# Kernel tuning notes

Measured on AMD Instinct MI355X. Metric: run time of the kernel, lower is better.

## Reference

```python
import jax, jax.numpy as jnp
import numpy as np

B, V, D = 4096, 10000, 512
ANNEAL = 1.0
EPSILON = 1.0  # regularization_type = 'OT'


def setup_inputs() -> dict:
    key = jax.random.key(0)
    ks = jax.random.split(key, 8)
    return {
        "recon_x": jax.random.normal(ks[0], (B, V), dtype=jnp.float32),
        "logits_rec": jax.random.normal(ks[1], (B, V), dtype=jnp.float32),
        "logits_text": jax.random.normal(ks[2], (B, V), dtype=jnp.float32),
        "x": jax.random.uniform(ks[3], (B, V), dtype=jnp.float32),
        "mu": jax.random.normal(ks[4], (B, D), dtype=jnp.float32),
        "logvar": jax.random.normal(ks[5], (B, D), dtype=jnp.float32),
        "prior_mu": jax.random.normal(ks[6], (B, D), dtype=jnp.float32),
        "prior_logvar": jax.random.normal(ks[7], (B, D), dtype=jnp.float32),
    }


def _bce(logits, x):
    # -mean_b(mean_v(log_softmax(logits,1) * x)) == global mean since both
    # reductions are plain means over the full [B, V] tensor.
    return -jnp.mean(jax.nn.log_softmax(logits, axis=1) * x)


def _kld(m, lv):
    return -0.5 * jnp.mean(1.0 + lv - m * m - jnp.exp(lv))


def reference(recon_x, logits_rec, logits_text, x, mu, logvar, prior_mu, prior_logvar):
    BCE_merged = _bce(recon_x, x)
    BCE_text = _bce(logits_text, x)
    BCE_rec = _bce(logits_rec, x)
    BCE = (BCE_merged + BCE_text + BCE_rec) / 3.0

    KLD1 = _kld(mu, logvar)
    KLD2 = _kld(prior_mu, prior_logvar)

    # Bures-Wasserstein^2 between diagonal Gaussians. The torch code builds
    # dense diag matrices and runs batched Cholesky/bmm; for diagonal covs
    # L1 = diag(sqrt(s1)), L1 @ C2 @ L1^T = diag(s1*s2), chol -> diag(sqrt(s1*s2)),
    # so the math reduces exactly to the O(d) closed form below.
    s1 = jnp.exp(logvar)          # [B, D]
    s2 = jnp.exp(prior_logvar)    # [B, D]
    mean_dist_sq = jnp.sum((mu - prior_mu) ** 2, axis=1)            # [B]
    trace_term = jnp.sum(s1 + s2 - 2.0 * jnp.sqrt(s1 * s2), axis=1)  # [B]
    wasserstein_loss = jnp.mean(mean_dist_sq + trace_term)

    l = BCE + ANNEAL / 2.0 * (KLD1 + KLD2) + EPSILON * wasserstein_loss
    return (l, BCE, wasserstein_loss, BCE_rec, BCE_text, BCE_merged)
```

## Files before the change

kernel.cpp:

```cpp
#include <hip/hip_runtime.h>

#define NROWS 4096
#define NCOLS 10000
#define DDIM  512

__device__ __forceinline__ float wave_reduce_sum(float v) {
    #pragma unroll
    for (int o = 32; o > 0; o >>= 1) v += __shfl_down(v, o, 64);
    return v;
}

__global__ __launch_bounds__(256) void bce_rows_kernel(
    const float4* __restrict__ merged,
    const float4* __restrict__ rec,
    const float4* __restrict__ text,
    const float4* __restrict__ xr,
    float* __restrict__ cm, float* __restrict__ ct, float* __restrict__ cr)
{
    const int row = blockIdx.x;
    const int nvec = NCOLS / 4;
    const size_t base = (size_t)row * nvec;

    float se_m = 0.f, se_t = 0.f, se_r = 0.f;
    float d_m = 0.f, d_t = 0.f, d_r = 0.f;
    float sx = 0.f;

    for (int i = threadIdx.x; i < nvec; i += 256) {
        const float4 xv = xr[base + i];
        const float4 mv = merged[base + i];
        const float4 tv = text[base + i];
        const float4 rv = rec[base + i];

        se_m += __expf(mv.x) + __expf(mv.y) + __expf(mv.z) + __expf(mv.w);
        se_t += __expf(tv.x) + __expf(tv.y) + __expf(tv.z) + __expf(tv.w);
        se_r += __expf(rv.x) + __expf(rv.y) + __expf(rv.z) + __expf(rv.w);

        d_m += mv.x * xv.x + mv.y * xv.y + mv.z * xv.z + mv.w * xv.w;
        d_t += tv.x * xv.x + tv.y * xv.y + tv.z * xv.z + tv.w * xv.w;
        d_r += rv.x * xv.x + rv.y * xv.y + rv.z * xv.z + rv.w * xv.w;

        sx += xv.x + xv.y + xv.z + xv.w;
    }

    __shared__ float sm[4][7];
    float vals[7] = {se_m, se_t, se_r, d_m, d_t, d_r, sx};
    #pragma unroll
    for (int k = 0; k < 7; ++k) vals[k] = wave_reduce_sum(vals[k]);

    const int wave = threadIdx.x >> 6;
    const int lane = threadIdx.x & 63;
    if (lane == 0) {
        #pragma unroll
        for (int k = 0; k < 7; ++k) sm[wave][k] = vals[k];
    }
    __syncthreads();

    if (threadIdx.x == 0) {
        float t[7];
        #pragma unroll
        for (int k = 0; k < 7; ++k)
            t[k] = sm[0][k] + sm[1][k] + sm[2][k] + sm[3][k];
        const float sumx = t[6];
        cm[row] = t[3] - __logf(t[0]) * sumx;
        ct[row] = t[4] - __logf(t[1]) * sumx;
        cr[row] = t[5] - __logf(t[2]) * sumx;
    }
}

__global__ __launch_bounds__(256) void kld_wass_kernel(
    const float4* __restrict__ mu, const float4* __restrict__ lv,
    const float4* __restrict__ pmu, const float4* __restrict__ plv,
    float* __restrict__ k1o, float* __restrict__ k2o, float* __restrict__ wo)
{
    const int nvec = NROWS * DDIM / 4;
    float k1 = 0.f, k2 = 0.f, wacc = 0.f;

    for (int i = blockIdx.x * 256 + threadIdx.x; i < nvec; i += gridDim.x * 256) {
        const float4 m  = mu[i];
        const float4 l  = lv[i];
        const float4 pm = pmu[i];
        const float4 pl = plv[i];

        #define KW_COMP(c)                                              \
        {                                                               \
            const float e1 = __expf(l.c);                               \
            const float e2 = __expf(pl.c);                              \
            k1 += 1.f + l.c - m.c * m.c - e1;                           \
            k2 += 1.f + pl.c - pm.c * pm.c - e2;                        \
            const float dm = m.c - pm.c;                                \
            wacc += dm * dm + e1 + e2 - 2.f * __expf(0.5f * (l.c + pl.c)); \
        }
        KW_COMP(x) KW_COMP(y) KW_COMP(z) KW_COMP(w)
        #undef KW_COMP
    }

    __shared__ float sm[4][3];
    k1 = wave_reduce_sum(k1);
    k2 = wave_reduce_sum(k2);
    wacc = wave_reduce_sum(wacc);
    const int wave = threadIdx.x >> 6;
    const int lane = threadIdx.x & 63;
    if (lane == 0) { sm[wave][0] = k1; sm[wave][1] = k2; sm[wave][2] = wacc; }
    __syncthreads();
    if (threadIdx.x == 0) {
        k1o[blockIdx.x] = sm[0][0] + sm[1][0] + sm[2][0] + sm[3][0];
        k2o[blockIdx.x] = sm[0][1] + sm[1][1] + sm[2][1] + sm[3][1];
        wo[blockIdx.x]  = sm[0][2] + sm[1][2] + sm[2][2] + sm[3][2];
    }
}

__global__ __launch_bounds__(256) void finalize_kernel(
    const float* __restrict__ cm, const float* __restrict__ ct,
    const float* __restrict__ cr, const float* __restrict__ k1p,
    const float* __restrict__ k2p, const float* __restrict__ wp,
    int nk, float* __restrict__ out)
{
    float sm_ = 0.f, st_ = 0.f, sr_ = 0.f;
    for (int i = threadIdx.x; i < NROWS; i += 256) {
        sm_ += cm[i]; st_ += ct[i]; sr_ += cr[i];
    }
    float s1 = 0.f, s2 = 0.f, sw = 0.f;
    for (int i = threadIdx.x; i < nk; i += 256) {
        s1 += k1p[i]; s2 += k2p[i]; sw += wp[i];
    }

    __shared__ float sh[4][6];
    float vals[6] = {sm_, st_, sr_, s1, s2, sw};
    #pragma unroll
    for (int k = 0; k < 6; ++k) vals[k] = wave_reduce_sum(vals[k]);
    const int wave = threadIdx.x >> 6;
    const int lane = threadIdx.x & 63;
    if (lane == 0) {
        #pragma unroll
        for (int k = 0; k < 6; ++k) sh[wave][k] = vals[k];
    }
    __syncthreads();

    if (threadIdx.x == 0) {
        float t[6];
        #pragma unroll
        for (int k = 0; k < 6; ++k)
            t[k] = sh[0][k] + sh[1][k] + sh[2][k] + sh[3][k];

        const float invBV = 1.f / ((float)NROWS * (float)NCOLS);
        const float BCE_merged = -t[0] * invBV;
        const float BCE_text   = -t[1] * invBV;
        const float BCE_rec    = -t[2] * invBV;
        const float BCE = (BCE_merged + BCE_text + BCE_rec) * (1.f / 3.f);

        const float invBD = 1.f / ((float)NROWS * (float)DDIM);
        const float KLD1 = -0.5f * t[3] * invBD;
        const float KLD2 = -0.5f * t[4] * invBD;
        const float wass = t[5] / (float)NROWS;

        const float l = BCE + 0.5f * (KLD1 + KLD2) + wass;

        out[0] = l;
        out[1] = BCE;
        out[2] = wass;
        out[3] = BCE_rec;
        out[4] = BCE_text;
        out[5] = BCE_merged;
    }
}

extern "C" void kernel_launch(void* const* d_in, const int* in_sizes, int n_in,
                              void* d_out, int out_size, void* d_ws, size_t ws_size,
                              hipStream_t stream) {
    const float4* recon_x      = (const float4*)d_in[0];
    const float4* logits_rec   = (const float4*)d_in[1];
    const float4* logits_text  = (const float4*)d_in[2];
    const float4* x            = (const float4*)d_in[3];
    const float4* mu           = (const float4*)d_in[4];
    const float4* logvar       = (const float4*)d_in[5];
    const float4* prior_mu     = (const float4*)d_in[6];
    const float4* prior_logvar = (const float4*)d_in[7];

    float* ws = (float*)d_ws;
    float* cm = ws;
    float* ct = ws + NROWS;
    float* cr = ws + 2 * NROWS;
    const int NK = 512;
    float* k1p = ws + 3 * NROWS;
    float* k2p = ws + 3 * NROWS + NK;
    float* wp  = ws + 3 * NROWS + 2 * NK;

    hipLaunchKernelGGL(kld_wass_kernel, dim3(NK), dim3(256), 0, stream,
                       mu, logvar, prior_mu, prior_logvar, k1p, k2p, wp);
    hipLaunchKernelGGL(bce_rows_kernel, dim3(NROWS), dim3(256), 0, stream,
                       recon_x, logits_rec, logits_text, x, cm, ct, cr);
    hipLaunchKernelGGL(finalize_kernel, dim3(1), dim3(256), 0, stream,
                       cm, ct, cr, k1p, k2p, wp, NK, (float*)d_out);
}
```

Baseline: 133.5 us.

## Fuse KLD/Wasserstein and BCE kernels into one launch with unrolled row loop

The separate KLD/Wasserstein reduction kernel is merged into the BCE row kernel: the first 256 blocks do the KLD/Wasserstein partials and the remaining blocks do one row each. This removes one kernel launch and lets the small reduction overlap with the large streaming work. The BCE loop is unrolled by two so each thread has eight float4 loads in flight. The KLD block count also drops from 512 to 256, giving each of those blocks more work.

```diff
diff --git a/kernel.cpp b/kernel.cpp
--- a/kernel.cpp
+++ b/kernel.cpp
@@ -3,6 +3,7 @@
 #define NROWS 4096
 #define NCOLS 10000
 #define DDIM  512
+#define NKLD  256
 
 __device__ __forceinline__ float wave_reduce_sum(float v) {
     #pragma unroll
@@ -10,14 +11,57 @@
     return v;
 }
 
-__global__ __launch_bounds__(256) void bce_rows_kernel(
+__global__ __launch_bounds__(256) void fused_main_kernel(
     const float4* __restrict__ merged,
     const float4* __restrict__ rec,
     const float4* __restrict__ text,
     const float4* __restrict__ xr,
-    float* __restrict__ cm, float* __restrict__ ct, float* __restrict__ cr)
+    const float4* __restrict__ mu, const float4* __restrict__ lv,
+    const float4* __restrict__ pmu, const float4* __restrict__ plv,
+    float* __restrict__ cm, float* __restrict__ ct, float* __restrict__ cr,
+    float* __restrict__ k1o, float* __restrict__ k2o, float* __restrict__ wo)
 {
-    const int row = blockIdx.x;
+    const int wave = threadIdx.x >> 6;
+    const int lane = threadIdx.x & 63;
+
+    if (blockIdx.x < NKLD) {
+        const int nvec = NROWS * DDIM / 4;
+        float k1 = 0.f, k2 = 0.f, wacc = 0.f;
+
+        for (int i = blockIdx.x * 256 + threadIdx.x; i < nvec; i += NKLD * 256) {
+            const float4 m  = mu[i];
+            const float4 l  = lv[i];
+            const float4 pm = pmu[i];
+            const float4 pl = plv[i];
+
+            #define KW_COMP(c)                                              \
+            {                                                               \
+                const float e1 = __expf(l.c);                               \
+                const float e2 = __expf(pl.c);                              \
+                k1 += 1.f + l.c - m.c * m.c - e1;                           \
+                k2 += 1.f + pl.c - pm.c * pm.c - e2;                        \
+                const float dm = m.c - pm.c;                                \
+                wacc += dm * dm + e1 + e2 - 2.f * __expf(0.5f * (l.c + pl.c)); \
+            }
+            KW_COMP(x) KW_COMP(y) KW_COMP(z) KW_COMP(w)
+            #undef KW_COMP
+        }
+
+        __shared__ float sm[4][3];
+        k1 = wave_reduce_sum(k1);
+        k2 = wave_reduce_sum(k2);
+        wacc = wave_reduce_sum(wacc);
+        if (lane == 0) { sm[wave][0] = k1; sm[wave][1] = k2; sm[wave][2] = wacc; }
+        __syncthreads();
+        if (threadIdx.x == 0) {
+            k1o[blockIdx.x] = sm[0][0] + sm[1][0] + sm[2][0] + sm[3][0];
+            k2o[blockIdx.x] = sm[0][1] + sm[1][1] + sm[2][1] + sm[3][1];
+            wo[blockIdx.x]  = sm[0][2] + sm[1][2] + sm[2][2] + sm[3][2];
+        }
+        return;
+    }
+
+    const int row = blockIdx.x - NKLD;
     const int nvec = NCOLS / 4;
     const size_t base = (size_t)row * nvec;
 
@@ -25,33 +69,46 @@
     float d_m = 0.f, d_t = 0.f, d_r = 0.f;
     float sx = 0.f;
 
-    for (int i = threadIdx.x; i < nvec; i += 256) {
+    #define BCE_BODY(xv, mv, tv, rv)                                          \
+    {                                                                         \
+        se_m += __expf(mv.x) + __expf(mv.y) + __expf(mv.z) + __expf(mv.w);    \
+        se_t += __expf(tv.x) + __expf(tv.y) + __expf(tv.z) + __expf(tv.w);    \
+        se_r += __expf(rv.x) + __expf(rv.y) + __expf(rv.z) + __expf(rv.w);    \
+        d_m += mv.x * xv.x + mv.y * xv.y + mv.z * xv.z + mv.w * xv.w;         \
+        d_t += tv.x * xv.x + tv.y * xv.y + tv.z * xv.z + tv.w * xv.w;         \
+        d_r += rv.x * xv.x + rv.y * xv.y + rv.z * xv.z + rv.w * xv.w;         \
+        sx  += xv.x + xv.y + xv.z + xv.w;                                     \
+    }
+
+    int i = threadIdx.x;
+    for (; i + 256 < nvec; i += 512) {
+        const float4 xv0 = xr[base + i];
+        const float4 mv0 = merged[base + i];
+        const float4 tv0 = text[base + i];
+        const float4 rv0 = rec[base + i];
+        const float4 xv1 = xr[base + i + 256];
+        const float4 mv1 = merged[base + i + 256];
+        const float4 tv1 = text[base + i + 256];
+        const float4 rv1 = rec[base + i + 256];
+        BCE_BODY(xv0, mv0, tv0, rv0)
+        BCE_BODY(xv1, mv1, tv1, rv1)
+    }
+    for (; i < nvec; i += 256) {
         const float4 xv = xr[base + i];
         const float4 mv = merged[base + i];
         const float4 tv = text[base + i];
         const float4 rv = rec[base + i];
-
-        se_m += __expf(mv.x) + __expf(mv.y) + __expf(mv.z) + __expf(mv.w);
-        se_t += __expf(tv.x) + __expf(tv.y) + __expf(tv.z) + __expf(tv.w);
-        se_r += __expf(rv.x) + __expf(rv.y) + __expf(rv.z) + __expf(rv.w);
-
-        d_m += mv.x * xv.x + mv.y * xv.y + mv.z * xv.z + mv.w * xv.w;
-        d_t += tv.x * xv.x + tv.y * xv.y + tv.z * xv.z + tv.w * xv.w;
-        d_r += rv.x * xv.x + rv.y * xv.y + rv.z * xv.z + rv.w * xv.w;
-
-        sx += xv.x + xv.y + xv.z + xv.w;
-    }
-
-    __shared__ float sm[4][7];
+        BCE_BODY(xv, mv, tv, rv)
+    }
+    #undef BCE_BODY
+
+    __shared__ float sm2[4][7];
     float vals[7] = {se_m, se_t, se_r, d_m, d_t, d_r, sx};
     #pragma unroll
     for (int k = 0; k < 7; ++k) vals[k] = wave_reduce_sum(vals[k]);
-
-    const int wave = threadIdx.x >> 6;
-    const int lane = threadIdx.x & 63;
     if (lane == 0) {
         #pragma unroll
-        for (int k = 0; k < 7; ++k) sm[wave][k] = vals[k];
+        for (int k = 0; k < 7; ++k) sm2[wave][k] = vals[k];
     }
     __syncthreads();
 
@@ -59,7 +116,7 @@
         float t[7];
         #pragma unroll
         for (int k = 0; k < 7; ++k)
-            t[k] = sm[0][k] + sm[1][k] + sm[2][k] + sm[3][k];
+            t[k] = sm2[0][k] + sm2[1][k] + sm2[2][k] + sm2[3][k];
         const float sumx = t[6];
         cm[row] = t[3] - __logf(t[0]) * sumx;
         ct[row] = t[4] - __logf(t[1]) * sumx;
@@ -67,60 +124,18 @@
     }
 }
 
-__global__ __launch_bounds__(256) void kld_wass_kernel(
-    const float4* __restrict__ mu, const float4* __restrict__ lv,
-    const float4* __restrict__ pmu, const float4* __restrict__ plv,
-    float* __restrict__ k1o, float* __restrict__ k2o, float* __restrict__ wo)
-{
-    const int nvec = NROWS * DDIM / 4;
-    float k1 = 0.f, k2 = 0.f, wacc = 0.f;
-
-    for (int i = blockIdx.x * 256 + threadIdx.x; i < nvec; i += gridDim.x * 256) {
-        const float4 m  = mu[i];
-        const float4 l  = lv[i];
-        const float4 pm = pmu[i];
-        const float4 pl = plv[i];
-
-        #define KW_COMP(c)                                              \
-        {                                                               \
-            const float e1 = __expf(l.c);                               \
-            const float e2 = __expf(pl.c);                              \
-            k1 += 1.f + l.c - m.c * m.c - e1;                           \
-            k2 += 1.f + pl.c - pm.c * pm.c - e2;                        \
-            const float dm = m.c - pm.c;                                \
-            wacc += dm * dm + e1 + e2 - 2.f * __expf(0.5f * (l.c + pl.c)); \
-        }
-        KW_COMP(x) KW_COMP(y) KW_COMP(z) KW_COMP(w)
-        #undef KW_COMP
-    }
-
-    __shared__ float sm[4][3];
-    k1 = wave_reduce_sum(k1);
-    k2 = wave_reduce_sum(k2);
-    wacc = wave_reduce_sum(wacc);
-    const int wave = threadIdx.x >> 6;
-    const int lane = threadIdx.x & 63;
-    if (lane == 0) { sm[wave][0] = k1; sm[wave][1] = k2; sm[wave][2] = wacc; }
-    __syncthreads();
-    if (threadIdx.x == 0) {
-        k1o[blockIdx.x] = sm[0][0] + sm[1][0] + sm[2][0] + sm[3][0];
-        k2o[blockIdx.x] = sm[0][1] + sm[1][1] + sm[2][1] + sm[3][1];
-        wo[blockIdx.x]  = sm[0][2] + sm[1][2] + sm[2][2] + sm[3][2];
-    }
-}
-
 __global__ __launch_bounds__(256) void finalize_kernel(
     const float* __restrict__ cm, const float* __restrict__ ct,
     const float* __restrict__ cr, const float* __restrict__ k1p,
     const float* __restrict__ k2p, const float* __restrict__ wp,
-    int nk, float* __restrict__ out)
+    float* __restrict__ out)
 {
     float sm_ = 0.f, st_ = 0.f, sr_ = 0.f;
     for (int i = threadIdx.x; i < NROWS; i += 256) {
         sm_ += cm[i]; st_ += ct[i]; sr_ += cr[i];
     }
     float s1 = 0.f, s2 = 0.f, sw = 0.f;
-    for (int i = threadIdx.x; i < nk; i += 256) {
+    for (int i = threadIdx.x; i < NKLD; i += 256) {
         s1 += k1p[i]; s2 += k2p[i]; sw += wp[i];
     }
 
@@ -180,15 +195,14 @@
     float* cm = ws;
     float* ct = ws + NROWS;
     float* cr = ws + 2 * NROWS;
-    const int NK = 512;
     float* k1p = ws + 3 * NROWS;
-    float* k2p = ws + 3 * NROWS + NK;
-    float* wp  = ws + 3 * NROWS + 2 * NK;
-
-    hipLaunchKernelGGL(kld_wass_kernel, dim3(NK), dim3(256), 0, stream,
-                       mu, logvar, prior_mu, prior_logvar, k1p, k2p, wp);
-    hipLaunchKernelGGL(bce_rows_kernel, dim3(NROWS), dim3(256), 0, stream,
-                       recon_x, logits_rec, logits_text, x, cm, ct, cr);
+    float* k2p = ws + 3 * NROWS + NKLD;
+    float* wp  = ws + 3 * NROWS + 2 * NKLD;
+
+    hipLaunchKernelGGL(fused_main_kernel, dim3(NKLD + NROWS), dim3(256), 0, stream,
+                       recon_x, logits_rec, logits_text, x,
+                       mu, logvar, prior_mu, prior_logvar,
+                       cm, ct, cr, k1p, k2p, wp);
     hipLaunchKernelGGL(finalize_kernel, dim3(1), dim3(256), 0, stream,
-                       cm, ct, cr, k1p, k2p, wp, NK, (float*)d_out);
-}
+                       cm, ct, cr, k1p, k2p, wp, (float*)d_out);
+}
```

New measurement: 128.9 us. 3.5% less time.
